# Kernel tuning notes

Hardware: AMD Instinct MI355X
Metric: run time of the kernel (lower is better)

## Reference

```python
import jax, jax.numpy as jnp
import numpy as np

NUM_CLASSES = 80
SCORE_THR = 0.2
NMS_THR = 0.3
MAX_PER_IMAGE = 100
TOPK_PER_CLASS = 100  # cap on pre-NMS candidates per (image, class); >= max_per_image
ANCHOR_MASK = [[6, 7, 8], [3, 4, 5], [0, 1, 2]]
COCO_ANCHORS = np.array([[10, 13], [16, 30], [33, 23], [30, 61], [62, 45],
                         [59, 119], [116, 90], [156, 198], [373, 326]], dtype=np.float32)


def yolo_head(feats, layer_anchors, num_classes, input_shape):
    # feats: [B, 3*(5+C), gh, gw]
    B = feats.shape[0]
    gh, gw = feats.shape[2], feats.shape[3]
    na = layer_anchors.shape[0]
    f = feats.reshape(B, na, num_classes + 5, gh, gw).transpose(0, 3, 4, 1, 2)  # [B,gh,gw,3,5+C]
    gy, gx = jnp.meshgrid(jnp.arange(gh), jnp.arange(gw), indexing='ij')
    grid = jnp.stack([gx, gy], axis=-1).astype(f.dtype)[None, :, :, None, :]  # [1,gh,gw,1,2]
    # literal translation: divide by tensor([gh, gw]) (square grids in practice)
    box_xy = (jax.nn.sigmoid(f[..., :2]) + grid) / jnp.array([gh, gw], f.dtype)
    box_wh = jnp.exp(f[..., 2:4]) * layer_anchors[None, None, None, :, :] / input_shape[None, None, None, None, :]
    conf = jax.nn.sigmoid(f[..., 4:5])
    probs = jax.nn.sigmoid(f[..., 5:])
    return box_xy, box_wh, conf, probs


def yolo_correct_boxes(box_xy, box_wh, input_shape, image_shape):
    box_yx = box_xy[..., ::-1]
    box_hw = box_wh[..., ::-1]
    new_shape = jnp.round(image_shape * jnp.min(input_shape / image_shape))
    offset = (input_shape - new_shape) / 2.0 / input_shape
    scale = input_shape / new_shape
    box_yx = (box_yx - offset) * scale
    box_hw = box_hw * scale
    mins = box_yx - box_hw / 2.0
    maxes = box_yx + box_hw / 2.0
    boxes = jnp.concatenate([mins, maxes], axis=-1)  # (ymin, xmin, ymax, xmax)
    return boxes * jnp.concatenate([image_shape, image_shape])


def decode_layer(feats, layer_anchors, input_shape, image_shape):
    box_xy, box_wh, conf, probs = yolo_head(feats, layer_anchors, NUM_CLASSES, input_shape)
    boxes = yolo_correct_boxes(box_xy, box_wh, input_shape, image_shape)  # [B,gh,gw,3,4]
    B = feats.shape[0]
    return boxes.reshape(B, -1, 4), (conf * probs).reshape(B, -1, NUM_CLASSES)


def pairwise_iou(b):
    # b: [K,4] (y1,x1,y2,x2)
    y1, x1, y2, x2 = b[:, 0], b[:, 1], b[:, 2], b[:, 3]
    area = jnp.maximum(y2 - y1, 0) * jnp.maximum(x2 - x1, 0)
    iy1 = jnp.maximum(y1[:, None], y1[None, :])
    ix1 = jnp.maximum(x1[:, None], x1[None, :])
    iy2 = jnp.minimum(y2[:, None], y2[None, :])
    ix2 = jnp.minimum(x2[:, None], x2[None, :])
    inter = jnp.maximum(iy2 - iy1, 0) * jnp.maximum(ix2 - ix1, 0)
    return inter / (area[:, None] + area[None, :] - inter + 1e-9)


def greedy_nms(boxes, valid):
    # boxes [K,4] sorted by descending score; valid [K] bool. Returns keep mask [K].
    K = boxes.shape[0]
    iou = jax.lax.stop_gradient(pairwise_iou(boxes))
    idx = jnp.arange(K)
    def body(i, sup):
        keep_i = valid[i] & (~sup[i])
        return sup | (keep_i & (iou[i] > NMS_THR) & (idx > i))
    sup = jax.lax.fori_loop(0, K, body, jnp.zeros((K,), bool))
    return valid & (~sup)


def setup_inputs() -> dict:
    key = jax.random.key(0)
    k0, k1, k2 = jax.random.split(key, 3)
    B, F = 16, 3 * (5 + NUM_CLASSES)
    feat0 = jax.random.normal(k0, (B, F, 19, 19), jnp.float32)
    feat1 = jax.random.normal(k1, (B, F, 38, 38), jnp.float32)
    feat2 = jax.random.normal(k2, (B, F, 76, 76), jnp.float32)
    anchors = jnp.asarray(COCO_ANCHORS)
    image_shape = jnp.array([480.0, 640.0], jnp.float32)
    return {"feat0": feat0, "feat1": feat1, "feat2": feat2,
            "anchors": anchors, "image_shape": image_shape}


def reference(feat0, feat1, feat2, anchors, image_shape):
    input_shape = jnp.array([feat0.shape[2] * 32, feat0.shape[3] * 32], jnp.float32)
    feats = [feat0, feat1, feat2]
    boxes_l, scores_l = [], []
    for l in range(3):
        b, s = decode_layer(feats[l], anchors[np.array(ANCHOR_MASK[l])], input_shape, image_shape)
        boxes_l.append(b)
        scores_l.append(s)
    boxes = jnp.concatenate(boxes_l, axis=1)    # [B,N,4]
    scores = jnp.concatenate(scores_l, axis=1)  # [B,N,C]
    B = scores.shape[0]
    sc = scores.transpose(0, 2, 1)              # [B,C,N]
    top_s, top_i = jax.lax.top_k(sc, TOPK_PER_CLASS)              # [B,C,K]
    top_b = jnp.take_along_axis(boxes[:, None, :, :], top_i[..., None], axis=2)  # [B,C,K,4]
    valid = top_s >= SCORE_THR
    keep = jax.vmap(jax.vmap(greedy_nms))(top_b, valid)           # [B,C,K]
    cand = jnp.where(keep, top_s, -1.0)
    flat_s = cand.reshape(B, -1)                 # [B, C*K]
    flat_b = top_b.reshape(B, -1, 4)
    sel_s, sel_i = jax.lax.top_k(flat_s, MAX_PER_IMAGE)           # [B,100]
    sel_b = jnp.take_along_axis(flat_b, sel_i[..., None], axis=1)  # [B,100,4]
    sel_c = (sel_i // TOPK_PER_CLASS).astype(jnp.float32)
    # dets: (ymin, xmin, ymax, xmax, score, class); score == -1 marks padding
    return jnp.concatenate([sel_b, sel_s[..., None], sel_c[..., None]], axis=-1)
```

## Files before the change

kernel.cpp:

```cpp
#include <hip/hip_runtime.h>
#include <hip/hip_bf16.h>


#define NTOT   22743
#define NCLS   80
#define TOPK   100
#define KPAD   22752
#define NVEC   2842
#define Q_L1   17328
#define Q_L0   21660
#define SCORE_THR 0.2f
#define NMS_THR   0.3f

__device__ __forceinline__ float sig_exact(float x) {
    return 1.0f / (1.0f + expf(-x));
}
__device__ __forceinline__ float sig_fast(float x) {
    return __builtin_amdgcn_rcpf(1.0f + __expf(-x));
}

__global__ __launch_bounds__(256) void k_decode(
    const float* __restrict__ f0, const float* __restrict__ f1,
    const float* __restrict__ f2, const float* __restrict__ anchors,
    const float* __restrict__ imshape, float4* __restrict__ boxes,
    float* __restrict__ conf_q, int total) {
    int gid = blockIdx.x * 256 + threadIdx.x;
    if (gid >= total) return;
    int b = gid / NTOT; int p = gid - b * NTOT;

    const float* f; int ghw, gw, l, off, a, s;
    if (p < 1083)      { f=f0; off=0;    ghw=361;  gw=19; l=0; int r=p;      a=r/361;  s=r-a*361;  }
    else if (p < 5415) { f=f1; off=1083; ghw=1444; gw=38; l=1; int r=p-1083; a=r/1444; s=r-a*1444; }
    else               { f=f2; off=5415; ghw=5776; gw=76; l=2; int r=p-5415; a=r/5776; s=r-a*5776; }
    int y = s / gw, x = s - y * gw;

    const float* q = f + ((size_t)(b * 255 + a * 85) * ghw + s);
    float tx = q[0], ty = q[ghw], tw = q[2*ghw], th = q[3*ghw], tc = q[4*ghw];

    int arow = (2 - l) * 3 + a;
    float aw = anchors[arow * 2], ah = anchors[arow * 2 + 1];
    float imh = imshape[0], imw = imshape[1];
    float gf = (float)gw;

    float bxx = (sig_exact(tx) + (float)x) / gf;
    float bxy = (sig_exact(ty) + (float)y) / gf;
    float bw  = expf(tw) * aw / 608.0f;
    float bh  = expf(th) * ah / 608.0f;

    float r  = fminf(608.0f / imh, 608.0f / imw);
    float nh = rintf(imh * r), nw = rintf(imw * r);
    float offy = (608.0f - nh) / 2.0f / 608.0f;
    float offx = (608.0f - nw) / 2.0f / 608.0f;
    float scy = 608.0f / nh, scx = 608.0f / nw;

    float cy = (bxy - offy) * scy;
    float cx = (bxx - offx) * scx;
    float hh = bh * scy, ww = bw * scx;

    int n = off + 3 * s + a;
    boxes[(size_t)b * NTOT + n] =
        make_float4((cy - hh / 2.0f) * imh, (cx - ww / 2.0f) * imw,
                    (cy + hh / 2.0f) * imh, (cx + ww / 2.0f) * imw);
    int qi = (l == 2) ? (a * 5776 + s)
           : (l == 1) ? (Q_L1 + a * 1444 + s)
                      : (Q_L0 + a * 361 + s);
    conf_q[(size_t)b * KPAD + qi] = sig_exact(tc);
}

#define SEG_A  346560
#define SEG_AB 433200
#define SEG_T  519840
__global__ __launch_bounds__(256) void k_score(
    const float* __restrict__ f0, const float* __restrict__ f1,
    const float* __restrict__ f2, const float* __restrict__ conf_q,
    unsigned short* __restrict__ keybuf, int total) {
    int gid = blockIdx.x * 256 + threadIdx.x;
    if (gid >= total) return;
    const int b = gid / SEG_T;
    const int w = gid - b * SEG_T;

    if (w < SEG_AB) {
        const float* f; int a, c, s, qbase, ghw;
        if (w < SEG_A) {
            a = w / 115520; int r = w - a * 115520;
            c = r / 1444;   s = (r - c * 1444) * 4;
            f = f2; ghw = 5776; qbase = a * 5776;
        } else {
            int t = w - SEG_A;
            a = t / 28880;  int r = t - a * 28880;
            c = r / 361;    s = (r - c * 361) * 4;
            f = f1; ghw = 1444; qbase = Q_L1 + a * 1444;
        }
        const float4 lg = *(const float4*)(f + ((size_t)(b * 255 + a * 85 + 5 + c) * ghw + s));
        const float4 cf = *(const float4*)(conf_q + (size_t)b * KPAD + qbase + s);
        ushort4 k;
        k.x = (unsigned short)(__float_as_uint(cf.x * sig_fast(lg.x)) >> 16);
        k.y = (unsigned short)(__float_as_uint(cf.y * sig_fast(lg.y)) >> 16);
        k.z = (unsigned short)(__float_as_uint(cf.z * sig_fast(lg.z)) >> 16);
        k.w = (unsigned short)(__float_as_uint(cf.w * sig_fast(lg.w)) >> 16);
        *(ushort4*)(keybuf + ((size_t)(b * NCLS + c)) * KPAD + qbase + s) = k;
    } else {
        int t = w - SEG_AB;
        int a = t / 28880;  int r = t - a * 28880;
        int c = r / 361;    int s = r - c * 361;
        int qi = Q_L0 + a * 361 + s;
        float lg = f0[((size_t)(b * 255 + a * 85 + 5 + c) * 361 + s)];
        float cf = conf_q[(size_t)b * KPAD + qi];
        keybuf[((size_t)(b * NCLS + c)) * KPAD + qi] =
            (unsigned short)(__float_as_uint(cf * sig_fast(lg)) >> 16);
    }
}

__device__ void find_pivot(unsigned* hist, int H, unsigned target,
                           unsigned* suf, unsigned* sh_p, unsigned* sh_above) {
    const int tid = threadIdx.x;
    const int per = H >> 8;
    if (tid < 256) {
        unsigned acc = 0;
        for (int u = 0; u < per; ++u) acc += hist[tid * per + u];
        suf[tid] = acc;
    }
    __syncthreads();
    for (int off = 1; off < 256; off <<= 1) {
        unsigned v = 0;
        if (tid < 256) v = (tid + off < 256) ? suf[tid + off] : 0u;
        __syncthreads();
        if (tid < 256) suf[tid] += v;
        __syncthreads();
    }
    if (tid < 256) {
        unsigned mysuf = suf[tid];
        unsigned nxt = (tid == 255) ? 0u : suf[tid + 1];
        if (mysuf >= target && nxt < target) {
            unsigned above = nxt;
            for (int h = tid * per + per - 1; h >= tid * per; --h) {
                unsigned c2 = above + hist[h];
                if (c2 >= target) { *sh_p = (unsigned)h; *sh_above = above; break; }
                above = c2;
            }
        }
    }
    __syncthreads();
}

__device__ __forceinline__ void collect_cand(
    int b, int c, int q, const float* __restrict__ f0,
    const float* __restrict__ f1, const float* __restrict__ f2,
    const float* __restrict__ conf_q, unsigned long long* buf,
    unsigned* sh_cnt) {
    int a, s, nbase, ghw;
    const float* f;
    if (q < Q_L1)      { a = q / 5776;  s = q - a * 5776;  f = f2; ghw = 5776; nbase = 5415; }
    else if (q < Q_L0) { int r = q - Q_L1; a = r / 1444; s = r - a * 1444; f = f1; ghw = 1444; nbase = 1083; }
    else               { int r = q - Q_L0; a = r / 361;  s = r - a * 361;  f = f0; ghw = 361;  nbase = 0;    }
    float t  = f[((size_t)(b * 255 + a * 85 + 5 + c)) * ghw + s];
    float cf = conf_q[(size_t)b * KPAD + q];
    float sce = cf * sig_exact(t);
    int n = nbase + 3 * s + a;
    unsigned slot = atomicAdd(sh_cnt, 1u);
    if (slot < 512)
        buf[slot] = (((unsigned long long)__float_as_uint(sce)) << 32)
                    | (unsigned)(~n);
}

__global__ __launch_bounds__(512, 8) void k_topk(
    const float* __restrict__ f0, const float* __restrict__ f1,
    const float* __restrict__ f2, const float* __restrict__ conf_q,
    const unsigned short* __restrict__ keybuf,
    const float4* __restrict__ boxes, float4* __restrict__ top_b,
    float* __restrict__ cand) {
    __shared__ unsigned int histp[4096];
    __shared__ unsigned long long buf[512];
    __shared__ unsigned int wsum[4];
    __shared__ float sb_y1[TOPK], sb_x1[TOPK], sb_y2[TOPK], sb_x2[TOPK], sb_s[TOPK];
    __shared__ unsigned int sh_p, sh_cnt;

    const int tid = threadIdx.x;
    const int row = blockIdx.x;
    const int b = row / NCLS, c = row - b * NCLS;
    const unsigned short* kr = keybuf + (size_t)row * KPAD;
    const uint4* kv = (const uint4*)kr;

    for (int i = tid; i < 4096; i += 512) histp[i] = 0;
    if (tid == 0) sh_cnt = 0;
    __syncthreads();

    uint4 v[6];
    bool  val[6];
    #pragma unroll
    for (int k = 0; k < 6; ++k) {
        int g = tid + k * 512;
        val[k] = (g < NVEC);
        v[k] = val[k] ? kv[g] : make_uint4(0, 0, 0, 0);
    }
    const bool hastail = (tid < NTOT - NVEC * 8);
    unsigned tailk = hastail ? (unsigned)kr[NVEC * 8 + tid] : 0u;

    #pragma unroll
    for (int k = 0; k < 6; ++k) if (val[k]) {
        unsigned ks[8] = { v[k].x & 0xFFFFu, v[k].x >> 16, v[k].y & 0xFFFFu, v[k].y >> 16,
                           v[k].z & 0xFFFFu, v[k].z >> 16, v[k].w & 0xFFFFu, v[k].w >> 16 };
        #pragma unroll
        for (int j = 0; j < 8; ++j)
            atomicAdd(&histp[ks[j] >> 2], 1u << (((ks[j] >> 1) & 1u) * 16));
    }
    if (hastail) atomicAdd(&histp[tailk >> 2], 1u << (((tailk >> 1) & 1u) * 16));
    __syncthreads();

    {
        const int lane = tid & 63;
        unsigned own = 0;
        if (tid < 256) {
            #pragma unroll
            for (int u = 0; u < 16; ++u) {
                unsigned w = histp[tid * 16 + u];
                own += (w & 0xFFFFu) + (w >> 16);
            }
        }
        unsigned acc = own;
        #pragma unroll
        for (int d = 1; d < 64; d <<= 1) {
            unsigned vv = __shfl_down(acc, d, 64);
            if (lane + d < 64) acc += vv;
        }
        if (tid < 256 && lane == 0) wsum[tid >> 6] = acc;
        __syncthreads();
        if (tid < 256) {
            unsigned tail = 0;
            for (int w2 = (tid >> 6) + 1; w2 < 4; ++w2) tail += wsum[w2];
            unsigned suft = acc + tail;
            unsigned nxt  = suft - own;
            if (suft >= TOPK && nxt < TOPK) {
                unsigned above = nxt;
                for (int bb = 31; bb >= 0; --bb) {
                    unsigned w = histp[tid * 16 + (bb >> 1)];
                    unsigned cnt = (bb & 1) ? (w >> 16) : (w & 0xFFFFu);
                    if (above + cnt >= TOPK) { sh_p = (unsigned)(tid * 32 + bb); break; }
                    above += cnt;
                }
            }
        }
        __syncthreads();
    }
    const unsigned kthr = sh_p > 0 ? ((sh_p - 1) << 1) : 0u;

    #pragma unroll
    for (int k = 0; k < 6; ++k) if (val[k]) {
        unsigned ks[8] = { v[k].x & 0xFFFFu, v[k].x >> 16, v[k].y & 0xFFFFu, v[k].y >> 16,
                           v[k].z & 0xFFFFu, v[k].z >> 16, v[k].w & 0xFFFFu, v[k].w >> 16 };
        #pragma unroll
        for (int j = 0; j < 8; ++j)
            if (ks[j] >= kthr)
                collect_cand(b, c, (tid + k * 512) * 8 + j, f0, f1, f2, conf_q, buf, &sh_cnt);
    }
    if (hastail && tailk >= kthr)
        collect_cand(b, c, NVEC * 8 + tid, f0, f1, f2, conf_q, buf, &sh_cnt);
    __syncthreads();

    const int M = (int)min(sh_cnt, 512u);
    if (tid < M) {
        unsigned long long mykey = buf[tid];
        int rank = 0;
        for (int j = 0; j < M; ++j) rank += (buf[j] > mykey);
        if (rank < TOPK) {
            int n = (int)(~(unsigned)mykey);
            float4 bx = boxes[(size_t)b * NTOT + n];
            sb_y1[rank] = bx.x; sb_x1[rank] = bx.y;
            sb_y2[rank] = bx.z; sb_x2[rank] = bx.w;
            sb_s[rank]  = __uint_as_float((unsigned)(mykey >> 32));
            top_b[(size_t)row * TOPK + rank] = bx;
        }
    }
    __syncthreads();

    if (tid < 64) {
        const int j0 = tid, j1 = tid + 64;
        const bool v1 = (j1 < TOPK);
        float y10 = sb_y1[j0], x10 = sb_x1[j0], y20 = sb_y2[j0], x20 = sb_x2[j0];
        float s0 = sb_s[j0];
        float y11 = v1 ? sb_y1[j1] : 0.f, x11 = v1 ? sb_x1[j1] : 0.f;
        float y21 = v1 ? sb_y2[j1] : 0.f, x21 = v1 ? sb_x2[j1] : 0.f;
        float s1 = v1 ? sb_s[j1] : -1.0f;
        float ar0 = fmaxf(y20 - y10, 0.f) * fmaxf(x20 - x10, 0.f);
        float ar1 = fmaxf(y21 - y11, 0.f) * fmaxf(x21 - x11, 0.f);
        int sup0 = 0, sup1 = 0;
        for (int i = 0; i < TOPK; ++i) {
            float yi1 = sb_y1[i], xi1 = sb_x1[i], yi2 = sb_y2[i], xi2 = sb_x2[i];
            float si = sb_s[i];
            int supi = (i < 64) ? __shfl(sup0, i, 64) : __shfl(sup1, i - 64, 64);
            bool keep_i = (si >= SCORE_THR) && (supi == 0);
            if (keep_i) {
                float ari = fmaxf(yi2 - yi1, 0.f) * fmaxf(xi2 - xi1, 0.f);
                if (j0 > i) {
                    float ty1 = fmaxf(yi1, y10), tx1 = fmaxf(xi1, x10);
                    float ty2 = fminf(yi2, y20), tx2 = fminf(xi2, x20);
                    float inter = fmaxf(ty2 - ty1, 0.f) * fmaxf(tx2 - tx1, 0.f);
                    float iou = inter / (ari + ar0 - inter + 1e-9f);
                    if (iou > NMS_THR) sup0 = 1;
                }
                if (v1 && j1 > i) {
                    float ty1 = fmaxf(yi1, y11), tx1 = fmaxf(xi1, x11);
                    float ty2 = fminf(yi2, y21), tx2 = fminf(xi2, x21);
                    float inter = fmaxf(ty2 - ty1, 0.f) * fmaxf(tx2 - tx1, 0.f);
                    float iou = inter / (ari + ar1 - inter + 1e-9f);
                    if (iou > NMS_THR) sup1 = 1;
                }
            }
        }
        cand[(size_t)row * TOPK + j0] = (s0 >= SCORE_THR && sup0 == 0) ? s0 : -1.0f;
        if (v1)
            cand[(size_t)row * TOPK + j1] = (s1 >= SCORE_THR && sup1 == 0) ? s1 : -1.0f;
    }
}

__global__ __launch_bounds__(256) void k_final(
    const float* __restrict__ cand, const float4* __restrict__ top_b,
    float* __restrict__ out) {
    __shared__ float cs[8000];
    __shared__ unsigned int hist[4096];
    __shared__ unsigned long long buf[512];
    __shared__ unsigned int suf[256];
    __shared__ unsigned int sh_kp, sh_p1, sh_above1, sh_p2, sh_above2, sh_cnt;

    const int tid = threadIdx.x, b = blockIdx.x;
    if (tid == 0) { sh_kp = 0; sh_cnt = 0; }
    for (int i = tid; i < 4096; i += 256) hist[i] = 0;
    __syncthreads();

    unsigned lk = 0;
    for (int i = tid; i < 8000; i += 256) {
        float v = cand[b * 8000 + i];
        cs[i] = v;
        if (v > -0.5f) lk++;
    }
    atomicAdd(&sh_kp, lk);
    __syncthreads();
    unsigned Kp = sh_kp;

    if (Kp >= TOPK) {
        for (int i = tid; i < 8000; i += 256)
            if (cs[i] > -0.5f) atomicAdd(&hist[__float_as_uint(cs[i]) >> 19], 1u);
        __syncthreads();
        find_pivot(hist, 2048, TOPK, suf, &sh_p1, &sh_above1);
        unsigned p1 = sh_p1, above1 = sh_above1;
        for (int i = tid; i < 4096; i += 256) hist[i] = 0;
        __syncthreads();
        for (int i = tid; i < 8000; i += 256) {
            float v = cs[i];
            if (v > -0.5f) {
                unsigned bits = __float_as_uint(v);
                if ((bits >> 19) == p1) atomicAdd(&hist[(bits >> 7) & 0xFFFu], 1u);
            }
        }
        __syncthreads();
        find_pivot(hist, 4096, TOPK - above1, suf, &sh_p2, &sh_above2);
        unsigned p2 = sh_p2;
        for (int i = tid; i < 8000; i += 256) {
            float v = cs[i];
            if (v > -0.5f) {
                unsigned bits = __float_as_uint(v);
                unsigned b1 = bits >> 19;
                if (b1 > p1 || (b1 == p1 && ((bits >> 7) & 0xFFFu) >= p2)) {
                    unsigned slot = atomicAdd(&sh_cnt, 1u);
                    if (slot < 512)
                        buf[slot] = (((unsigned long long)bits) << 32) | (unsigned)(~i);
                }
            }
        }
    } else {
        for (int i = tid; i < 8000; i += 256) {
            float v = cs[i];
            if (v > -0.5f) {
                unsigned slot = atomicAdd(&sh_cnt, 1u);
                buf[slot] = (((unsigned long long)__float_as_uint(v)) << 32) | (unsigned)(~i);
            }
        }
        __syncthreads();
        if (tid == 0) {
            unsigned need = TOPK - Kp, got = 0;
            for (int i = 0; i < 8000 && got < need; ++i)
                if (cs[i] <= -0.5f) { buf[Kp + got] = (unsigned)(~i); got++; }
        }
    }
    __syncthreads();

    const int M2 = (Kp >= TOPK) ? (int)min(sh_cnt, 512u) : (int)TOPK;
    for (int i = tid; i < M2; i += 256) {
        unsigned long long key = buf[i];
        int rank = 0;
        for (int j = 0; j < M2; ++j) rank += (buf[j] > key);
        if (rank < TOPK) {
            int fi = (int)(~(unsigned)key);
            int c = fi / TOPK; int kk = fi - c * TOPK;
            float4 bb = top_b[((size_t)b * NCLS + c) * TOPK + kk];
            int base = (b * TOPK + rank) * 6;
            out[base + 0] = bb.x; out[base + 1] = bb.y;
            out[base + 2] = bb.z; out[base + 3] = bb.w;
            out[base + 4] = cs[fi]; out[base + 5] = (float)c;
        }
    }
}

extern "C" void kernel_launch(void* const* d_in, const int* in_sizes, int n_in,
                              void* d_out, int out_size, void* d_ws, size_t ws_size,
                              hipStream_t stream) {
    (void)n_in; (void)out_size; (void)ws_size;
    const float* f0      = (const float*)d_in[0];
    const float* f1      = (const float*)d_in[1];
    const float* f2      = (const float*)d_in[2];
    const float* anchors = (const float*)d_in[3];
    const float* imshape = (const float*)d_in[4];
    const int B = in_sizes[0] / (255 * 19 * 19);

    char* ws = (char*)d_ws;
    size_t o = 0;
    unsigned short* keybuf = (unsigned short*)(ws + o);
    o += (size_t)B * NCLS * KPAD * sizeof(unsigned short);
    float4* boxes  = (float4*)(ws + o); o += (size_t)B * NTOT * sizeof(float4);
    float*  conf_q = (float*)(ws + o);  o += (size_t)B * KPAD * sizeof(float);
    float4* top_b  = (float4*)(ws + o); o += (size_t)B * NCLS * TOPK * sizeof(float4);
    float*  cand   = (float*)(ws + o);  o += (size_t)B * NCLS * TOPK * sizeof(float);
    float*  out    = (float*)d_out;

    const int total = B * NTOT;
    k_decode<<<(total + 255) / 256, 256, 0, stream>>>(f0, f1, f2, anchors, imshape,
                                                      boxes, conf_q, total);
    const int stotal = B * SEG_T;
    k_score<<<(stotal + 255) / 256, 256, 0, stream>>>(f0, f1, f2, conf_q,
                                                      keybuf, stotal);
    k_topk<<<B * NCLS, 512, 0, stream>>>(f0, f1, f2, conf_q, keybuf, boxes,
                                         top_b, cand);
    k_final<<<B, 256, 0, stream>>>(cand, top_b, out);
}
```

Before: 265.7 us.

## Split per-class NMS out of top-k kernel into a wave-per-row kernel

The top-k kernel no longer runs greedy NMS. Previously only one 64-lane wave of each 512-thread block did that serial 100-step loop while the rest of the block sat idle. The kernel now writes the top scores and boxes to global memory, and a new k_nms kernel handles four rows per 256-thread block. Each wave keeps its boxes in registers and broadcasts them with wave shuffles instead of LDS arrays. The cost is an extra kernel launch plus a global write and read of the top-k scores and boxes.

After: 266.7 us. About the same (+0.4%).

```diff
diff --git a/kernel.cpp b/kernel.cpp
--- a/kernel.cpp
+++ b/kernel.cpp
@@ -167,12 +167,11 @@
     const float* __restrict__ f0, const float* __restrict__ f1,
     const float* __restrict__ f2, const float* __restrict__ conf_q,
     const unsigned short* __restrict__ keybuf,
-    const float4* __restrict__ boxes, float4* __restrict__ top_b,
-    float* __restrict__ cand) {
+    const float4* __restrict__ boxes, float* __restrict__ top_s,
+    float4* __restrict__ top_b) {
     __shared__ unsigned int histp[4096];
     __shared__ unsigned long long buf[512];
     __shared__ unsigned int wsum[4];
-    __shared__ float sb_y1[TOPK], sb_x1[TOPK], sb_y2[TOPK], sb_x2[TOPK], sb_s[TOPK];
     __shared__ unsigned int sh_p, sh_cnt;
 
     const int tid = threadIdx.x;
@@ -264,53 +263,61 @@
         for (int j = 0; j < M; ++j) rank += (buf[j] > mykey);
         if (rank < TOPK) {
             int n = (int)(~(unsigned)mykey);
-            float4 bx = boxes[(size_t)b * NTOT + n];
-            sb_y1[rank] = bx.x; sb_x1[rank] = bx.y;
-            sb_y2[rank] = bx.z; sb_x2[rank] = bx.w;
-            sb_s[rank]  = __uint_as_float((unsigned)(mykey >> 32));
-            top_b[(size_t)row * TOPK + rank] = bx;
-        }
-    }
-    __syncthreads();
-
-    if (tid < 64) {
-        const int j0 = tid, j1 = tid + 64;
-        const bool v1 = (j1 < TOPK);
-        float y10 = sb_y1[j0], x10 = sb_x1[j0], y20 = sb_y2[j0], x20 = sb_x2[j0];
-        float s0 = sb_s[j0];
-        float y11 = v1 ? sb_y1[j1] : 0.f, x11 = v1 ? sb_x1[j1] : 0.f;
-        float y21 = v1 ? sb_y2[j1] : 0.f, x21 = v1 ? sb_x2[j1] : 0.f;
-        float s1 = v1 ? sb_s[j1] : -1.0f;
-        float ar0 = fmaxf(y20 - y10, 0.f) * fmaxf(x20 - x10, 0.f);
-        float ar1 = fmaxf(y21 - y11, 0.f) * fmaxf(x21 - x11, 0.f);
-        int sup0 = 0, sup1 = 0;
-        for (int i = 0; i < TOPK; ++i) {
-            float yi1 = sb_y1[i], xi1 = sb_x1[i], yi2 = sb_y2[i], xi2 = sb_x2[i];
-            float si = sb_s[i];
-            int supi = (i < 64) ? __shfl(sup0, i, 64) : __shfl(sup1, i - 64, 64);
-            bool keep_i = (si >= SCORE_THR) && (supi == 0);
-            if (keep_i) {
-                float ari = fmaxf(yi2 - yi1, 0.f) * fmaxf(xi2 - xi1, 0.f);
-                if (j0 > i) {
-                    float ty1 = fmaxf(yi1, y10), tx1 = fmaxf(xi1, x10);
-                    float ty2 = fminf(yi2, y20), tx2 = fminf(xi2, x20);
-                    float inter = fmaxf(ty2 - ty1, 0.f) * fmaxf(tx2 - tx1, 0.f);
-                    float iou = inter / (ari + ar0 - inter + 1e-9f);
-                    if (iou > NMS_THR) sup0 = 1;
-                }
-                if (v1 && j1 > i) {
-                    float ty1 = fmaxf(yi1, y11), tx1 = fmaxf(xi1, x11);
-                    float ty2 = fminf(yi2, y21), tx2 = fminf(xi2, x21);
-                    float inter = fmaxf(ty2 - ty1, 0.f) * fmaxf(tx2 - tx1, 0.f);
-                    float iou = inter / (ari + ar1 - inter + 1e-9f);
-                    if (iou > NMS_THR) sup1 = 1;
-                }
-            }
-        }
-        cand[(size_t)row * TOPK + j0] = (s0 >= SCORE_THR && sup0 == 0) ? s0 : -1.0f;
-        if (v1)
-            cand[(size_t)row * TOPK + j1] = (s1 >= SCORE_THR && sup1 == 0) ? s1 : -1.0f;
-    }
+            top_s[(size_t)row * TOPK + rank] = __uint_as_float((unsigned)(mykey >> 32));
+            top_b[(size_t)row * TOPK + rank] = boxes[(size_t)b * NTOT + n];
+        }
+    }
+}
+
+__global__ __launch_bounds__(256) void k_nms(
+    const float* __restrict__ top_s, const float4* __restrict__ top_b,
+    float* __restrict__ cand) {
+    const int lane = threadIdx.x & 63;
+    const int row  = blockIdx.x * 4 + (threadIdx.x >> 6);
+    const float4* bb = top_b + (size_t)row * TOPK;
+    const float*  ss = top_s + (size_t)row * TOPK;
+
+    const int j0 = lane, j1 = lane + 64;
+    const bool v1 = (j1 < TOPK);
+    float4 B0 = bb[j0];
+    float  s0 = ss[j0];
+    float4 B1 = v1 ? bb[j1] : make_float4(0.f, 0.f, 0.f, 0.f);
+    float  s1 = v1 ? ss[j1] : -1.0f;
+    float ar0 = fmaxf(B0.z - B0.x, 0.f) * fmaxf(B0.w - B0.y, 0.f);
+    float ar1 = fmaxf(B1.z - B1.x, 0.f) * fmaxf(B1.w - B1.y, 0.f);
+    int sup0 = 0, sup1 = 0;
+
+    for (int i = 0; i < TOPK; ++i) {
+        const int src = i & 63;
+        const bool hi = (i >= 64);
+        float yi1 = __shfl(hi ? B1.x : B0.x, src, 64);
+        float xi1 = __shfl(hi ? B1.y : B0.y, src, 64);
+        float yi2 = __shfl(hi ? B1.z : B0.z, src, 64);
+        float xi2 = __shfl(hi ? B1.w : B0.w, src, 64);
+        float si  = __shfl(hi ? s1   : s0,   src, 64);
+        int  supi = __shfl(hi ? sup1 : sup0, src, 64);
+        bool keep_i = (si >= SCORE_THR) && (supi == 0);
+        if (keep_i) {
+            float ari = fmaxf(yi2 - yi1, 0.f) * fmaxf(xi2 - xi1, 0.f);
+            if (j0 > i) {
+                float ty1 = fmaxf(yi1, B0.x), tx1 = fmaxf(xi1, B0.y);
+                float ty2 = fminf(yi2, B0.z), tx2 = fminf(xi2, B0.w);
+                float inter = fmaxf(ty2 - ty1, 0.f) * fmaxf(tx2 - tx1, 0.f);
+                float iou = inter / (ari + ar0 - inter + 1e-9f);
+                if (iou > NMS_THR) sup0 = 1;
+            }
+            if (v1 && j1 > i) {
+                float ty1 = fmaxf(yi1, B1.x), tx1 = fmaxf(xi1, B1.y);
+                float ty2 = fminf(yi2, B1.z), tx2 = fminf(xi2, B1.w);
+                float inter = fmaxf(ty2 - ty1, 0.f) * fmaxf(tx2 - tx1, 0.f);
+                float iou = inter / (ari + ar1 - inter + 1e-9f);
+                if (iou > NMS_THR) sup1 = 1;
+            }
+        }
+    }
+    cand[(size_t)row * TOPK + j0] = (s0 >= SCORE_THR && sup0 == 0) ? s0 : -1.0f;
+    if (v1)
+        cand[(size_t)row * TOPK + j1] = (s1 >= SCORE_THR && sup1 == 0) ? s1 : -1.0f;
 }
 
 __global__ __launch_bounds__(256) void k_final(
@@ -418,6 +425,7 @@
     o += (size_t)B * NCLS * KPAD * sizeof(unsigned short);
     float4* boxes  = (float4*)(ws + o); o += (size_t)B * NTOT * sizeof(float4);
     float*  conf_q = (float*)(ws + o);  o += (size_t)B * KPAD * sizeof(float);
+    float*  top_s  = (float*)(ws + o);  o += (size_t)B * NCLS * TOPK * sizeof(float);
     float4* top_b  = (float4*)(ws + o); o += (size_t)B * NCLS * TOPK * sizeof(float4);
     float*  cand   = (float*)(ws + o);  o += (size_t)B * NCLS * TOPK * sizeof(float);
     float*  out    = (float*)d_out;
@@ -429,6 +437,7 @@
     k_score<<<(stotal + 255) / 256, 256, 0, stream>>>(f0, f1, f2, conf_q,
                                                       keybuf, stotal);
     k_topk<<<B * NCLS, 512, 0, stream>>>(f0, f1, f2, conf_q, keybuf, boxes,
-                                         top_b, cand);
+                                         top_s, top_b);
+    k_nms<<<(B * NCLS) / 4, 256, 0, stream>>>(top_s, top_b, cand);
     k_final<<<B, 256, 0, stream>>>(cand, top_b, out);
 }
```
